# Kernel tuning notes

Hardware: AMD Instinct MI355X
Metric: run time of the kernel (lower is better)

## Reference

```python
import jax, jax.numpy as jnp
import numpy as np

N_E = 8192
E_DIM = 64
BETA = 0.25


def setup_inputs() -> dict:
    key = jax.random.key(0)
    k_z, k_e = jax.random.split(key)
    z = jax.random.normal(k_z, (16, E_DIM, 64, 64), dtype=jnp.float32)  # b c h w
    # nn.Embedding weight init: uniform(-1/n_e, 1/n_e)
    embedding = jax.random.uniform(
        k_e, (N_E, E_DIM), dtype=jnp.float32, minval=-1.0 / N_E, maxval=1.0 / N_E
    )
    return {"z": z, "embedding": embedding}


def reference(z, embedding):
    # b c h w -> b h w c
    zc = jnp.transpose(z, (0, 2, 3, 1))
    zf = zc.reshape(-1, embedding.shape[1])  # [N, d]
    # squared euclidean distances: ||z||^2 + ||e||^2 - 2 z.e
    d = (
        jnp.sum(zf * zf, axis=1, keepdims=True)
        + jnp.sum(embedding * embedding, axis=1)
        - 2.0 * jnp.einsum("nd,kd->nk", zf, embedding)
    )  # [N, K]
    min_encoding_indices = jnp.argmin(d, axis=1)  # [N]
    z_q = jnp.take(embedding, min_encoding_indices, axis=0).reshape(zc.shape)
    # legacy=True loss
    loss = jnp.mean((jax.lax.stop_gradient(z_q) - zc) ** 2) + BETA * jnp.mean(
        (z_q - jax.lax.stop_gradient(zc)) ** 2
    )
    # straight-through estimator
    z_q = zc + jax.lax.stop_gradient(z_q - zc)
    z_q = jnp.transpose(z_q, (0, 3, 1, 2))  # b h w c -> b c h w
    return z_q, loss, min_encoding_indices
```

## Files before the change

kernel.cpp:

```cpp
#include <hip/hip_runtime.h>

#define NTOT 65536
#define KC   8192
#define DV   64
#define ZQN  4194304
#define NSPL 4
#define KSL  2048
#define NTILE 16
#define CAP2 16
#define SLA  44u
#define SLE  40u

typedef unsigned int u32;
typedef unsigned long long u64;
typedef unsigned short ushort;
typedef short short8 __attribute__((ext_vector_type(8)));
typedef float float4v __attribute__((ext_vector_type(4)));

__device__ __forceinline__ short f2bf(float x) {
    u32 u = __float_as_uint(x);
    u32 r = (u + 0x7fffu + ((u >> 16) & 1u)) >> 16;
    return (short)r;
}

__global__ __launch_bounds__(256) void vq_prep(
    const float* __restrict__ emb, float* __restrict__ nrm,
    u32* __restrict__ cnt, double* __restrict__ lacc,
    ushort* __restrict__ ebs) {
    const int tid = blockIdx.x * 256 + threadIdx.x;
    const int t = tid >> 10, r = tid & 1023;
    const int s = r >> 7, r2 = r & 127, h = r2 >> 6, l = r2 & 63;
    const int q = l >> 4, c = l & 15;
    const float* src = emb + (size_t)((t * 128 + s * 16 + c) * 64 + h * 32 + q * 8);
    short8 v;
#pragma unroll
    for (int j = 0; j < 8; ++j) v[j] = f2bf(src[j]);
    *reinterpret_cast<short8*>(ebs + (size_t)tid * 8) = v;
    cnt[tid] = 0u;
    if (tid < KC) {
        double sacc = 0.0;
#pragma unroll
        for (int d = 0; d < DV; ++d) {
            double x = (double)emb[(size_t)tid * DV + d];
            sacc = fma(x, x, sacc);
        }
        nrm[tid] = (float)sacc;
    }
    if (tid == 0) *lacc = 0.0;
}

__global__ __launch_bounds__(256)
void vq_pass(const float* __restrict__ z, const ushort* __restrict__ ebs,
             u32* __restrict__ cnt, u32* __restrict__ cand) {
    const int tid = threadIdx.x;
    const int lane = tid & 63;
    const int nblk = blockIdx.x & 255, ks = blockIdx.x >> 8;
    const int nb = nblk * 256 + (tid >> 6) * 64;
    const int col = lane & 15, quad = lane >> 4;
    const int nlo = nb + col;

    short8 zf[4][2];
#pragma unroll
    for (int ns = 0; ns < 4; ++ns) {
        int n = nlo + ns * 16;
        const float* zp = z + (size_t)(n >> 12) * 262144 + (n & 4095);
#pragma unroll
        for (int t2 = 0; t2 < 2; ++t2)
#pragma unroll
            for (int j = 0; j < 8; ++j)
                zf[ns][t2][j] = f2bf(zp[(size_t)(t2 * 32 + quad * 8 + j) * 4096]);
    }

    u32 r0[4] = {0, 0, 0, 0}, r1[4] = {0, 0, 0, 0}, r2[4] = {0, 0, 0, 0};
    const char* gs = (const char*)ebs + (size_t)ks * (KSL * DV * 2);

    for (int t = 0; t < NTILE; ++t) {
#pragma unroll
        for (int g2 = 0; g2 < 4; ++g2) {
            const char* tb = gs + t * 16384 + g2 * 4096;
            short8 a00 = *reinterpret_cast<const short8*>(tb + lane * 16);
            short8 a01 = *reinterpret_cast<const short8*>(tb + 1024 + lane * 16);
            short8 a10 = *reinterpret_cast<const short8*>(tb + 2048 + lane * 16);
            short8 a11 = *reinterpret_cast<const short8*>(tb + 3072 + lane * 16);
            const u32 lowc = 0x80000000u + (u32)(((t * 4 + g2) << 2) | quad);
#pragma unroll
            for (int ns = 0; ns < 4; ++ns) {
                float4v acc0 = {0.f, 0.f, 0.f, 0.f};
                float4v acc1 = {0.f, 0.f, 0.f, 0.f};
                acc0 = __builtin_amdgcn_mfma_f32_16x16x32_bf16(a00, zf[ns][0], acc0, 0, 0, 0);
                acc0 = __builtin_amdgcn_mfma_f32_16x16x32_bf16(a01, zf[ns][1], acc0, 0, 0, 0);
                acc1 = __builtin_amdgcn_mfma_f32_16x16x32_bf16(a10, zf[ns][0], acc1, 0, 0, 0);
                acc1 = __builtin_amdgcn_mfma_f32_16x16x32_bf16(a11, zf[ns][1], acc1, 0, 0, 0);
                float q0 = fmaxf(fmaxf(acc0[0], acc0[1]), acc0[2]);
                float q1 = fmaxf(fmaxf(acc0[3], acc1[0]), acc1[1]);
                float q2 = fmaxf(fmaxf(acc1[2], acc1[3]), q0);
                float m  = fmaxf(q2, q1);
                u32 e = ((u32)(int)(m * 1048576.0f) << 16) + lowc;
                u32 x  = min(r0[ns], e);
                r0[ns] = max(r0[ns], e);
                u32 y  = min(r1[ns], x);
                r1[ns] = max(r1[ns], x);
                r2[ns] = max(r2[ns], y);
            }
        }
    }

#pragma unroll
    for (int ns = 0; ns < 4; ++ns) {
        u32 m = r0[ns];
        m = max(m, __shfl_xor(m, 16));
        m = max(m, __shfl_xor(m, 32));
        const u32 thr = (m & 0xffff0000u) - (SLA << 16);
        const int n = nlo + ns * 16;
        const u32 tag = (u32)ks << 8;
        if (r0[ns] >= thr) {
            u32 p = atomicAdd(&cnt[n], 1u);
            if (p < CAP2) cand[(size_t)n * CAP2 + p] = r0[ns] | tag;
        }
        if (r1[ns] >= thr) {
            u32 p = atomicAdd(&cnt[n], 1u);
            if (p < CAP2) cand[(size_t)n * CAP2 + p] = r1[ns] | tag;
        }
        if (r2[ns] >= thr) {
            u32 p = atomicAdd(&cnt[n], 1u);
            if (p < CAP2) cand[(size_t)n * CAP2 + p] = r2[ns] | tag;
        }
    }
}

__global__ __launch_bounds__(256) void vq_e1(
    const float* __restrict__ z, const float* __restrict__ emb,
    const float* __restrict__ nrm, const u32* __restrict__ cnt,
    const u32* __restrict__ cand, int* __restrict__ idxw,
    float* __restrict__ out) {
    __shared__ float zs[64][20];
    __shared__ float As[16];
    const int tid = threadIdx.x;
    const int n0 = blockIdx.x * 16;
    const int b = n0 >> 12, hw0 = n0 & 4095;
    {
        const float* zb = z + (size_t)b * 262144 + hw0;
        const int d = tid >> 2, i4 = (tid & 3) * 4;
        float4 v = *reinterpret_cast<const float4*>(zb + (size_t)d * 4096 + i4);
        *reinterpret_cast<float4*>(&zs[d][i4]) = v;
    }
    __syncthreads();

    const int li  = tid >> 4;
    const int n   = n0 + li;
    const int sub = tid & 15;
    const int dh  = sub & 1;
    const int j4  = (sub >> 1) & 3;
    const int st  = sub >> 3;

    if (sub == 0) {
        double ad = 0.0;
#pragma unroll
        for (int d = 0; d < DV; ++d) {
            double x = (double)zs[d][li];
            ad = fma(x, x, ad);
        }
        As[li] = (float)ad;
    }

    u32 c = min(cnt[n], (u32)CAP2);
    u32 emax = 0u;
    for (u32 j = 0; j < c; ++j) {
        u32 e = cand[(size_t)n * CAP2 + j];
        if (e > emax) emax = e;
    }
    const u32 ethr = (emax & 0xffff0000u) - (SLE << 16);

    float zh[32];
#pragma unroll
    for (int i = 0; i < 16; ++i) {
        zh[2 * i]     = zs[4 * i + 2 * dh][li];
        zh[2 * i + 1] = zs[4 * i + 2 * dh + 1][li];
    }

    u32 surv[3]; int nsv = 0;
    for (u32 j = (u32)j4; j < c; j += 4) {
        u32 e = cand[(size_t)n * CAP2 + j];
        if (e >= ethr) surv[nsv++] = e;
    }

    __syncthreads();
    const float A = As[li];

    float dmin = 1e30f;
    int kmin = 0x7fffffff;
    for (int i = 0; i < nsv; ++i) {
        u32 e = surv[i];
        int s   = (int)(e >> 8) & 3;
        int grp = (int)(e >> 2) & 63;
        int q   = (int)e & 3;
        int base = s * KSL + grp * 32 + q * 4 + st * 16;
#pragma unroll
        for (int r = 0; r < 4; ++r) {
            const int k = base + r;
            const float* ep = emb + (size_t)k * DV + 2 * dh;
            float dd;
            {
#pragma clang fp contract(off)
                float a0 = 0.f, a1 = 0.f;
#pragma unroll
                for (int i2 = 0; i2 < 4; ++i2) {
                    float2 v0 = *reinterpret_cast<const float2*>(ep + 16 * i2 + 0);
                    float2 v1 = *reinterpret_cast<const float2*>(ep + 16 * i2 + 4);
                    float2 v2 = *reinterpret_cast<const float2*>(ep + 16 * i2 + 8);
                    float2 v3 = *reinterpret_cast<const float2*>(ep + 16 * i2 + 12);
                    a0 = (zh[(i2*4+0)*2] * v0.x) + ((zh[(i2*4+1)*2] * v1.x) +
                         ((zh[(i2*4+2)*2] * v2.x) + ((zh[(i2*4+3)*2] * v3.x) + a0)));
                    a1 = (zh[(i2*4+0)*2+1] * v0.y) + ((zh[(i2*4+1)*2+1] * v1.y) +
                         ((zh[(i2*4+2)*2+1] * v2.y) + ((zh[(i2*4+3)*2+1] * v3.y) + a1)));
                }
                float sh = a0 + a1;
                float ot = __shfl_xor(sh, 1, 64);
                float dot = sh + ot;
                dd  = (A + nrm[k]) - (2.0f * dot);
            }
            if (dd < dmin || (dd == dmin && k < kmin)) { dmin = dd; kmin = k; }
        }
    }
    u64 key = ((u64)__float_as_uint(dmin) << 32) | (u32)kmin;
    u64 o1 = __shfl_xor(key, 1, 64); if (o1 < key) key = o1;
    u64 o2 = __shfl_xor(key, 2, 64); if (o2 < key) key = o2;
    u64 o4 = __shfl_xor(key, 4, 64); if (o4 < key) key = o4;
    u64 o8 = __shfl_xor(key, 8, 64); if (o8 < key) key = o8;
    if (sub == 0) {
        int km = (int)(key & 0xffffffffu);
        idxw[n] = km;
        out[(size_t)ZQN + 1 + n] = (float)km;
    }
}

__global__ __launch_bounds__(256) void vq_e2(
    const float* __restrict__ z, const float* __restrict__ emb,
    const int* __restrict__ idxw, float* __restrict__ out,
    double* __restrict__ lacc) {
    __shared__ double red[4];
    const int tid = threadIdx.x;
    const int n = blockIdx.x * 64 + (tid & 63);
    const int part = tid >> 6;
    const int b = n >> 12, hw = n & 4095;
    const int kmin = idxw[n];
    const float* zp = z + (size_t)b * 262144 + hw;
    const float4* er4 = (const float4*)(emb + (size_t)kmin * DV + part * 16);
    double lsum = 0.0;
#pragma unroll
    for (int i4 = 0; i4 < 4; ++i4) {
        float4 ev = er4[i4];
#pragma unroll
        for (int u = 0; u < 4; ++u) {
            int c = part * 16 + i4 * 4 + u;
            float v = (u == 0) ? ev.x : (u == 1) ? ev.y : (u == 2) ? ev.z : ev.w;
            out[(size_t)b * 262144 + (size_t)c * 4096 + hw] = v;
            double dv = (double)v - (double)zp[(size_t)c * 4096];
            lsum = fma(dv, dv, lsum);
        }
    }
#pragma unroll
    for (int off = 32; off > 0; off >>= 1)
        lsum += __shfl_down(lsum, off, 64);
    if ((tid & 63) == 0) red[tid >> 6] = lsum;
    __syncthreads();
    if (tid == 0)
        atomicAdd(lacc, red[0] + red[1] + red[2] + red[3]);
}

__global__ void vq_fin(const double* __restrict__ lacc, float* __restrict__ out) {
    if (threadIdx.x == 0)
        out[ZQN] = (float)(1.25 * (*lacc) / (double)ZQN);
}

extern "C" void kernel_launch(void* const* d_in, const int* in_sizes, int n_in,
                              void* d_out, int out_size, void* d_ws, size_t ws_size,
                              hipStream_t stream) {
    const float* z   = (const float*)d_in[0];
    const float* emb = (const float*)d_in[1];
    float* out = (float*)d_out;

    ushort* ebs  = (ushort*)d_out;
    u32*    cand = (u32*)((char*)d_out + 1048576);
    double* lacc   = (double*)d_ws;
    float*  nrm    = (float*)((char*)d_ws + 64);
    u32*    cnt    = (u32*)((char*)d_ws + 32832);
    int*    idxw   = (int*)((char*)d_ws + 294976);

    vq_prep<<<256, 256, 0, stream>>>(emb, nrm, cnt, lacc, ebs);
    vq_pass<<<NSPL * 256, 256, 0, stream>>>(z, ebs, cnt, cand);
    vq_e1<<<4096, 256, 0, stream>>>(z, emb, nrm, cnt, cand, idxw, out);
    vq_e2<<<1024, 256, 0, stream>>>(z, emb, idxw, out, lacc);
    vq_fin<<<1, 64, 0, stream>>>(lacc, out);
}
```

Baseline: 215.6 us.

## Switch coarse VQ distance pass to 32x32x16 bf16 MFMA with new codebook layout

Replaces the 16x16x32 MFMA tiling in the candidate-pruning pass with 32x32x16 bf16 MFMAs over 32 rows × 32 codes. The bf16 codebook pre-layout in the prep kernel and the candidate index decoding in the refine kernel change to match the new accumulator layout. Fewer, larger MFMAs and a single cross-lane shuffle aim to cut instruction-issue and reduction overhead. It also pins occupancy to 4 waves per EU. The 16-register accumulator raises register pressure, and the candidate tag encoding must stay consistent across kernels.

```diff
diff --git a/kernel.cpp b/kernel.cpp
--- a/kernel.cpp
+++ b/kernel.cpp
@@ -6,7 +6,6 @@
 #define ZQN  4194304
 #define NSPL 4
 #define KSL  2048
-#define NTILE 16
 #define CAP2 16
 #define SLA  44u
 #define SLE  40u
@@ -15,7 +14,7 @@
 typedef unsigned long long u64;
 typedef unsigned short ushort;
 typedef short short8 __attribute__((ext_vector_type(8)));
-typedef float float4v __attribute__((ext_vector_type(4)));
+typedef float float16v __attribute__((ext_vector_type(16)));
 
 __device__ __forceinline__ short f2bf(float x) {
     u32 u = __float_as_uint(x);
@@ -28,10 +27,10 @@
     u32* __restrict__ cnt, double* __restrict__ lacc,
     ushort* __restrict__ ebs) {
     const int tid = blockIdx.x * 256 + threadIdx.x;
-    const int t = tid >> 10, r = tid & 1023;
-    const int s = r >> 7, r2 = r & 127, h = r2 >> 6, l = r2 & 63;
-    const int q = l >> 4, c = l & 15;
-    const float* src = emb + (size_t)((t * 128 + s * 16 + c) * 64 + h * 32 + q * 8);
+    const int l = tid & 63, kc = (tid >> 6) & 3, cg = tid >> 8;
+    const int code = cg * 32 + (l & 31);
+    const int d = kc * 16 + (l >> 5) * 8;
+    const float* src = emb + (size_t)code * 64 + d;
     short8 v;
 #pragma unroll
     for (int j = 0; j < 8; ++j) v[j] = f2bf(src[j]);
@@ -40,8 +39,8 @@
     if (tid < KC) {
         double sacc = 0.0;
 #pragma unroll
-        for (int d = 0; d < DV; ++d) {
-            double x = (double)emb[(size_t)tid * DV + d];
+        for (int dd = 0; dd < DV; ++dd) {
+            double x = (double)emb[(size_t)tid * DV + dd];
             sacc = fma(x, x, sacc);
         }
         nrm[tid] = (float)sacc;
@@ -49,81 +48,94 @@
     if (tid == 0) *lacc = 0.0;
 }
 
-__global__ __launch_bounds__(256)
+__global__ __launch_bounds__(256) __attribute__((amdgpu_waves_per_eu(4, 4)))
 void vq_pass(const float* __restrict__ z, const ushort* __restrict__ ebs,
              u32* __restrict__ cnt, u32* __restrict__ cand) {
     const int tid = threadIdx.x;
     const int lane = tid & 63;
     const int nblk = blockIdx.x & 255, ks = blockIdx.x >> 8;
     const int nb = nblk * 256 + (tid >> 6) * 64;
-    const int col = lane & 15, quad = lane >> 4;
-    const int nlo = nb + col;
-
-    short8 zf[4][2];
-#pragma unroll
-    for (int ns = 0; ns < 4; ++ns) {
-        int n = nlo + ns * 16;
+    const int col = lane & 31, hi = lane >> 5, hi8 = hi * 8;
+
+    short8 zf[2][4];
+#pragma unroll
+    for (int nsub = 0; nsub < 2; ++nsub) {
+        int n = nb + nsub * 32 + col;
         const float* zp = z + (size_t)(n >> 12) * 262144 + (n & 4095);
 #pragma unroll
-        for (int t2 = 0; t2 < 2; ++t2)
+        for (int kc = 0; kc < 4; ++kc)
 #pragma unroll
             for (int j = 0; j < 8; ++j)
-                zf[ns][t2][j] = f2bf(zp[(size_t)(t2 * 32 + quad * 8 + j) * 4096]);
-    }
-
-    u32 r0[4] = {0, 0, 0, 0}, r1[4] = {0, 0, 0, 0}, r2[4] = {0, 0, 0, 0};
+                zf[nsub][kc][j] = f2bf(zp[(size_t)(kc * 16 + hi8 + j) * 4096]);
+    }
+
+    u32 r0[2] = {0, 0}, r1[2] = {0, 0}, r2[2] = {0, 0};
     const char* gs = (const char*)ebs + (size_t)ks * (KSL * DV * 2);
 
-    for (int t = 0; t < NTILE; ++t) {
+    for (int t = 0; t < 16; ++t) {
 #pragma unroll
         for (int g2 = 0; g2 < 4; ++g2) {
-            const char* tb = gs + t * 16384 + g2 * 4096;
-            short8 a00 = *reinterpret_cast<const short8*>(tb + lane * 16);
-            short8 a01 = *reinterpret_cast<const short8*>(tb + 1024 + lane * 16);
-            short8 a10 = *reinterpret_cast<const short8*>(tb + 2048 + lane * 16);
-            short8 a11 = *reinterpret_cast<const short8*>(tb + 3072 + lane * 16);
-            const u32 lowc = 0x80000000u + (u32)(((t * 4 + g2) << 2) | quad);
-#pragma unroll
-            for (int ns = 0; ns < 4; ++ns) {
-                float4v acc0 = {0.f, 0.f, 0.f, 0.f};
-                float4v acc1 = {0.f, 0.f, 0.f, 0.f};
-                acc0 = __builtin_amdgcn_mfma_f32_16x16x32_bf16(a00, zf[ns][0], acc0, 0, 0, 0);
-                acc0 = __builtin_amdgcn_mfma_f32_16x16x32_bf16(a01, zf[ns][1], acc0, 0, 0, 0);
-                acc1 = __builtin_amdgcn_mfma_f32_16x16x32_bf16(a10, zf[ns][0], acc1, 0, 0, 0);
-                acc1 = __builtin_amdgcn_mfma_f32_16x16x32_bf16(a11, zf[ns][1], acc1, 0, 0, 0);
-                float q0 = fmaxf(fmaxf(acc0[0], acc0[1]), acc0[2]);
-                float q1 = fmaxf(fmaxf(acc0[3], acc1[0]), acc1[1]);
-                float q2 = fmaxf(fmaxf(acc1[2], acc1[3]), q0);
-                float m  = fmaxf(q2, q1);
-                u32 e = ((u32)(int)(m * 1048576.0f) << 16) + lowc;
-                u32 x  = min(r0[ns], e);
-                r0[ns] = max(r0[ns], e);
-                u32 y  = min(r1[ns], x);
-                r1[ns] = max(r1[ns], x);
-                r2[ns] = max(r2[ns], y);
+            const int g = t * 4 + g2;
+            const char* tb = gs + g * 4096;
+            short8 a0 = *reinterpret_cast<const short8*>(tb + lane * 16);
+            short8 a1 = *reinterpret_cast<const short8*>(tb + 1024 + lane * 16);
+            short8 a2 = *reinterpret_cast<const short8*>(tb + 2048 + lane * 16);
+            short8 a3 = *reinterpret_cast<const short8*>(tb + 3072 + lane * 16);
+            const u32 lowc0 = 0x80000000u + (u32)((g << 2) | hi);
+            const u32 lowc1 = lowc0 + 2u;
+#pragma unroll
+            for (int nsub = 0; nsub < 2; ++nsub) {
+                float16v acc = {0.f,0.f,0.f,0.f,0.f,0.f,0.f,0.f,
+                                0.f,0.f,0.f,0.f,0.f,0.f,0.f,0.f};
+                acc = __builtin_amdgcn_mfma_f32_32x32x16_bf16(a0, zf[nsub][0], acc, 0, 0, 0);
+                acc = __builtin_amdgcn_mfma_f32_32x32x16_bf16(a1, zf[nsub][1], acc, 0, 0, 0);
+                acc = __builtin_amdgcn_mfma_f32_32x32x16_bf16(a2, zf[nsub][2], acc, 0, 0, 0);
+                acc = __builtin_amdgcn_mfma_f32_32x32x16_bf16(a3, zf[nsub][3], acc, 0, 0, 0);
+                {
+                    float q0 = fmaxf(fmaxf(acc[0], acc[1]), acc[2]);
+                    float q1 = fmaxf(fmaxf(acc[3], acc[4]), acc[5]);
+                    float q2 = fmaxf(fmaxf(acc[6], acc[7]), q0);
+                    float m  = fmaxf(q2, q1);
+                    u32 e = ((u32)(int)(m * 1048576.0f) << 16) + lowc0;
+                    u32 x  = min(r0[nsub], e);
+                    r0[nsub] = max(r0[nsub], e);
+                    u32 y  = min(r1[nsub], x);
+                    r1[nsub] = max(r1[nsub], x);
+                    r2[nsub] = max(r2[nsub], y);
+                }
+                {
+                    float q0 = fmaxf(fmaxf(acc[8], acc[9]), acc[10]);
+                    float q1 = fmaxf(fmaxf(acc[11], acc[12]), acc[13]);
+                    float q2 = fmaxf(fmaxf(acc[14], acc[15]), q0);
+                    float m  = fmaxf(q2, q1);
+                    u32 e = ((u32)(int)(m * 1048576.0f) << 16) + lowc1;
+                    u32 x  = min(r0[nsub], e);
+                    r0[nsub] = max(r0[nsub], e);
+                    u32 y  = min(r1[nsub], x);
+                    r1[nsub] = max(r1[nsub], x);
+                    r2[nsub] = max(r2[nsub], y);
+                }
             }
         }
     }
 
 #pragma unroll
-    for (int ns = 0; ns < 4; ++ns) {
-        u32 m = r0[ns];
-        m = max(m, __shfl_xor(m, 16));
-        m = max(m, __shfl_xor(m, 32));
+    for (int nsub = 0; nsub < 2; ++nsub) {
+        u32 m = max(r0[nsub], (u32)__shfl_xor(r0[nsub], 32, 64));
         const u32 thr = (m & 0xffff0000u) - (SLA << 16);
-        const int n = nlo + ns * 16;
+        const int n = nb + nsub * 32 + col;
         const u32 tag = (u32)ks << 8;
-        if (r0[ns] >= thr) {
+        if (r0[nsub] >= thr) {
             u32 p = atomicAdd(&cnt[n], 1u);
-            if (p < CAP2) cand[(size_t)n * CAP2 + p] = r0[ns] | tag;
-        }
-        if (r1[ns] >= thr) {
+            if (p < CAP2) cand[(size_t)n * CAP2 + p] = r0[nsub] | tag;
+        }
+        if (r1[nsub] >= thr) {
             u32 p = atomicAdd(&cnt[n], 1u);
-            if (p < CAP2) cand[(size_t)n * CAP2 + p] = r1[ns] | tag;
-        }
-        if (r2[ns] >= thr) {
+            if (p < CAP2) cand[(size_t)n * CAP2 + p] = r1[nsub] | tag;
+        }
+        if (r2[nsub] >= thr) {
             u32 p = atomicAdd(&cnt[n], 1u);
-            if (p < CAP2) cand[(size_t)n * CAP2 + p] = r2[ns] | tag;
+            if (p < CAP2) cand[(size_t)n * CAP2 + p] = r2[nsub] | tag;
         }
     }
 }
@@ -193,8 +205,9 @@
         u32 e = surv[i];
         int s   = (int)(e >> 8) & 3;
         int grp = (int)(e >> 2) & 63;
-        int q   = (int)e & 3;
-        int base = s * KSL + grp * 32 + q * 4 + st * 16;
+        int cb  = (int)(e >> 1) & 1;
+        int hi  = (int)e & 1;
+        int base = s * KSL + grp * 32 + cb * 16 + hi * 4 + st * 8;
 #pragma unroll
         for (int r = 0; r < 4; ++r) {
             const int k = base + r;
```

Result: no change. 211.6 us (median of 2 runs) (-1.9%).
